# Kernel tuning notes

Hardware: AMD Instinct MI355X
Metric: run time of the kernel (lower is better)

Reference implementation:

```python
import jax, jax.numpy as jnp
import numpy as np

D_MODEL = 768
N_HEADS = 12
HEAD_DIM = D_MODEL // N_HEADS


def setup_inputs() -> dict:
    key = jax.random.key(0)
    ks = jax.random.split(key, 9)
    B, S = 2, 2048
    x = jax.random.normal(ks[0], (B, S, D_MODEL), dtype=jnp.float32)
    s = 1.0 / np.sqrt(D_MODEL)
    Wq = jax.random.normal(ks[1], (D_MODEL, D_MODEL), dtype=jnp.float32) * s
    bq = jax.random.normal(ks[2], (D_MODEL,), dtype=jnp.float32) * 0.01
    Wk = jax.random.normal(ks[3], (D_MODEL, D_MODEL), dtype=jnp.float32) * s
    bk = jax.random.normal(ks[4], (D_MODEL,), dtype=jnp.float32) * 0.01
    Wv = jax.random.normal(ks[5], (D_MODEL, D_MODEL), dtype=jnp.float32) * s
    bv = jax.random.normal(ks[6], (D_MODEL,), dtype=jnp.float32) * 0.01
    Wo = jax.random.normal(ks[7], (D_MODEL, D_MODEL), dtype=jnp.float32) * s
    bo = jax.random.normal(ks[8], (D_MODEL,), dtype=jnp.float32) * 0.01
    return {"x": x, "Wq": Wq, "bq": bq, "Wk": Wk, "bk": bk,
            "Wv": Wv, "bv": bv, "Wo": Wo, "bo": bo}


def reference(x, Wq, bq, Wk, bk, Wv, bv, Wo, bo):
    B, S, _ = x.shape
    H, Dh = N_HEADS, HEAD_DIM
    # Projections (torch Linear: x @ W.T + b; here W stored as [in, out])
    q = (x @ Wq + bq).reshape(B, S, H, Dh)
    k = (x @ Wk + bk).reshape(B, S, H, Dh)
    v = (x @ Wv + bv).reshape(B, S, H, Dh)
    scale = 1.0 / jnp.sqrt(jnp.float32(Dh))
    # NOTE: source applies no causal mask despite the class name.
    scores = jnp.einsum('bqhd,bkhd->bhqk', q, k) * scale
    attn = jax.nn.softmax(scores, axis=-1)
    out = jnp.einsum('bhqk,bkhd->bqhd', attn, v).reshape(B, S, H * Dh)
    return out @ Wo + bo
```

## Files before the change

kernel.cpp:

```cpp
#include <hip/hip_runtime.h>

typedef unsigned short u16;
typedef __fp16 halfx2 __attribute__((ext_vector_type(2)));
typedef __fp16 halfx8 __attribute__((ext_vector_type(8)));
typedef float floatx4 __attribute__((ext_vector_type(4)));
typedef unsigned short u16x4 __attribute__((ext_vector_type(4)));
typedef unsigned short u16x8 __attribute__((ext_vector_type(8)));

#define D_MODEL 768
#define NH 12
#define DH 64
#define SEQ 2048
#define BATCH 2
#define MTOK 4096
#define DQKV 2304

__device__ __forceinline__ u16 f2h(float f) {
    __fp16 h = (__fp16)f;
    return __builtin_bit_cast(u16, h);
}

__device__ __forceinline__ void gload_lds16(const void* g, void* l) {
    __builtin_amdgcn_global_load_lds(
        (const __attribute__((address_space(1))) void*)g,
        (__attribute__((address_space(3))) void*)l, 16, 0, 0);
}


__global__ __launch_bounds__(256) void wprep_kernel(const float* __restrict__ Wq, const float* __restrict__ Wk,
                                                    const float* __restrict__ Wv, const float* __restrict__ Wo,
                                                    const float* __restrict__ x,
                                                    u16* __restrict__ WqkvT, u16* __restrict__ WoT,
                                                    u16* __restrict__ xh) {
    __shared__ u16 t[64][72];
    int bid = blockIdx.x;
    int tid = threadIdx.x;
    if (bid >= 576) {
        int idx = (bid - 576) * 2048 + tid * 8;
        float4 v0 = *(const float4*)(x + idx);
        float4 v1 = *(const float4*)(x + idx + 4);
        union { u16x8 u; halfx2 h[4]; } pk;
        pk.h[0] = __builtin_amdgcn_cvt_pkrtz(v0.x, v0.y);
        pk.h[1] = __builtin_amdgcn_cvt_pkrtz(v0.z, v0.w);
        pk.h[2] = __builtin_amdgcn_cvt_pkrtz(v1.x, v1.y);
        pk.h[3] = __builtin_amdgcn_cvt_pkrtz(v1.z, v1.w);
        *(u16x8*)(xh + idx) = pk.u;
        return;
    }
    int z = bid / 144;
    int t2 = bid % 144;
    int k0 = (t2 / 12) * 64, n0 = (t2 % 12) * 64;
    const float* W = (z == 0) ? Wq : (z == 1) ? Wk : (z == 2) ? Wv : Wo;
    u16* dst = (z < 3) ? (WqkvT + (size_t)z * 768 * 768) : WoT;
#pragma unroll
    for (int p = 0; p < 16; ++p) {
        int idx = p * 256 + tid;
        int kr = idx >> 6, nc = idx & 63;
        t[kr][nc] = f2h(W[(size_t)(k0 + kr) * 768 + n0 + nc]);
    }
    __syncthreads();
#pragma unroll
    for (int p = 0; p < 16; ++p) {
        int idx = p * 256 + tid;
        int nr = idx >> 6, kc = idx & 63;
        dst[(size_t)(n0 + nr) * 768 + k0 + kc] = t[kc][nr];
    }
}


__global__ __launch_bounds__(256) void gemm_qkv(const u16* __restrict__ xh, const u16* __restrict__ Bt,
                                                const float* __restrict__ bq, const float* __restrict__ bk,
                                                const float* __restrict__ bv,
                                                u16* __restrict__ qP, u16* __restrict__ kP,
                                                u16* __restrict__ vTout) {
    const int tid = threadIdx.x;
    const int wid = tid >> 6;
    const int lane = tid & 63;
    const int qd = lane >> 4;
    const int l15 = lane & 15;

    const int tn = blockIdx.x * 128;
    const int tm = blockIdx.y * 64;
    const int wm = (wid >> 1) * 32;
    const int wn = (wid & 1) * 64;

    __shared__ alignas(16) u16 As[64 * 64];
    __shared__ alignas(16) u16 Bs[128 * 64];

    floatx4 acc[2][4];
#pragma unroll
    for (int i = 0; i < 2; ++i)
#pragma unroll
        for (int j = 0; j < 4; ++j) acc[i][j] = (floatx4)(0.0f);

    const u16* Ag[2];
#pragma unroll
    for (int rd = 0; rd < 2; ++rd) {
        int s = rd * 256 + tid;
        int r = s >> 3, bl = (s & 7) ^ (r & 7);
        Ag[rd] = xh + (size_t)(tm + r) * 768 + bl * 8;
    }
    const u16* Bg[4];
#pragma unroll
    for (int rd = 0; rd < 4; ++rd) {
        int s = rd * 256 + tid;
        int r = s >> 3, bl = (s & 7) ^ (r & 7);
        Bg[rd] = Bt + (size_t)(tn + r) * 768 + bl * 8;
    }

    for (int kb = 0; kb < 768; kb += 64) {
        __syncthreads();
#pragma unroll
        for (int rd = 0; rd < 2; ++rd)
            gload_lds16(Ag[rd] + kb, As + (size_t)(rd * 256 + tid) * 8);
#pragma unroll
        for (int rd = 0; rd < 4; ++rd)
            gload_lds16(Bg[rd] + kb, Bs + (size_t)(rd * 256 + tid) * 8);
        __syncthreads();

#pragma unroll
        for (int ks = 0; ks < 2; ++ks) {
            halfx8 af[2], bf[4];
#pragma unroll
            for (int i = 0; i < 2; ++i) {
                int r = wm + i * 16 + l15;
                af[i] = *(const halfx8*)(As + r * 64 + (((ks * 4 + qd) ^ (r & 7)) * 8));
            }
#pragma unroll
            for (int j = 0; j < 4; ++j) {
                int r2 = wn + j * 16 + l15;
                bf[j] = *(const halfx8*)(Bs + r2 * 64 + (((ks * 4 + qd) ^ (r2 & 7)) * 8));
            }
#pragma unroll
            for (int i = 0; i < 2; ++i)
#pragma unroll
                for (int j = 0; j < 4; ++j)
                    acc[i][j] = __builtin_amdgcn_mfma_f32_16x16x32_f16(af[i], bf[j], acc[i][j], 0, 0, 0);
        }
    }

    const float cscale = 0.125f * 1.44269504088896340736f;
    const int rgn = (tn < 768) ? 0 : (tn < 1536) ? 1 : 2;
    const float* bsrc = (rgn == 0) ? bq : (rgn == 1) ? bk : bv;
#pragma unroll
    for (int j = 0; j < 4; ++j) {
        int col = tn + wn + j * 16 + l15;
        int cl = col - rgn * 768;
        float bvv = bsrc[cl];
        int h = cl >> 6, d = cl & 63;
#pragma unroll
        for (int i = 0; i < 2; ++i) {
            int row0 = tm + wm + i * 16 + qd * 4;
            int b = row0 >> 11, s0 = row0 & 2047;
            u16x4 pk;
#pragma unroll
            for (int r = 0; r < 4; ++r) {
                float v = acc[i][j][r] + bvv;
                if (rgn == 0) v *= cscale;
                pk[r] = f2h(v);
            }
            if (rgn == 2) {
                *(u16x4*)(vTout + ((size_t)(b * NH + h) * 64 + d) * SEQ + s0) = pk;
            } else {
                u16* dst = (rgn == 0) ? qP : kP;
#pragma unroll
                for (int r = 0; r < 4; ++r)
                    dst[((size_t)(b * NH + h) * SEQ + s0 + r) * DH + d] = pk[r];
            }
        }
    }
}


__global__ __launch_bounds__(256, 3) void attn_kernel(const u16* __restrict__ qP, const u16* __restrict__ kP,
                                                      const u16* __restrict__ vT, u16* __restrict__ attn) {
    const int tid = threadIdx.x;
    const int wid = tid >> 6;
    const int lane = tid & 63;
    const int qd = lane >> 4;
    const int l15 = lane & 15;

    const int bh = blockIdx.x;
    const int b = bh / NH, h = bh % NH;
    const int q0 = blockIdx.y * 64;

    __shared__ alignas(16) u16 smem[13312];
    u16* qlds = smem;
    u16* ps = smem + 4096 + wid * 2304;

#pragma unroll
    for (int ks = 0; ks < 2; ++ks) {
        halfx8 qv = *(const halfx8*)(qP + (size_t)(bh * SEQ + q0 + wid * 16 + l15) * DH + ks * 32 + qd * 8);
        *(halfx8*)(qlds + (size_t)((ks * 4 + wid) * 64 + lane) * 8) = qv;
    }
    __syncthreads();

    auto AQ = [&](int jn, int ks) -> halfx8 {
        return *(const halfx8*)(qlds + (size_t)((ks * 4 + jn) * 64 + lane) * 8);
    };

    floatx4 o[4][4];
#pragma unroll
    for (int ip = 0; ip < 4; ++ip)
#pragma unroll
        for (int jn = 0; jn < 4; ++jn) o[ip][jn] = (floatx4)(0.0f);
    float lsum[4] = {0.0f, 0.0f, 0.0f, 0.0f};

    const u16* kbase = kP + (size_t)(bh * SEQ + wid * 32 + l15) * DH + qd * 8;
    const u16* vbase = vT + (size_t)(bh * 64 + l15) * SEQ + wid * 32 + qd * 8;

    floatx4 sc[2][4];
    {
        halfx8 ak0[2][2];
#pragma unroll
        for (int mi = 0; mi < 2; ++mi)
#pragma unroll
            for (int ks = 0; ks < 2; ++ks)
                ak0[mi][ks] = *(const halfx8*)(kbase + (size_t)(mi * 16) * DH + ks * 32);
#pragma unroll
        for (int jn = 0; jn < 4; ++jn) {
            halfx8 a0 = AQ(jn, 0), a1 = AQ(jn, 1);
#pragma unroll
            for (int mi = 0; mi < 2; ++mi) {
                floatx4 z = (floatx4)(0.0f);
                z = __builtin_amdgcn_mfma_f32_16x16x32_f16(ak0[mi][0], a0, z, 0, 0, 0);
                sc[mi][jn] = __builtin_amdgcn_mfma_f32_16x16x32_f16(ak0[mi][1], a1, z, 0, 0, 0);
            }
        }
    }

    for (int kt = 0; kt < 16; ++kt) {
        const int kt1 = (kt + 1) & 15;

        halfx8 akn[2][2];
#pragma unroll
        for (int mi = 0; mi < 2; ++mi)
#pragma unroll
            for (int ks = 0; ks < 2; ++ks)
                akn[mi][ks] = *(const halfx8*)(kbase + (size_t)(kt1 * 128 + mi * 16) * DH + ks * 32);
        halfx8 avc[4];
#pragma unroll
        for (int ip = 0; ip < 4; ++ip)
            avc[ip] = *(const halfx8*)(vbase + (size_t)(ip * 16) * SEQ + kt * 128);

#pragma unroll
        for (int mi = 0; mi < 2; ++mi)
#pragma unroll
            for (int jn = 0; jn < 4; ++jn) {
                float p0 = __builtin_amdgcn_exp2f(sc[mi][jn][0]);
                float p1 = __builtin_amdgcn_exp2f(sc[mi][jn][1]);
                float p2 = __builtin_amdgcn_exp2f(sc[mi][jn][2]);
                float p3 = __builtin_amdgcn_exp2f(sc[mi][jn][3]);
                lsum[jn] += (p0 + p1) + (p2 + p3);
                union { u16x4 u; halfx2 h[2]; } pk;
                pk.h[0] = __builtin_amdgcn_cvt_pkrtz(p0, p1);
                pk.h[1] = __builtin_amdgcn_cvt_pkrtz(p2, p3);
                *(u16x4*)(ps + (jn * 16 + l15) * 36 + mi * 16 + qd * 4) = pk.u;
            }

        __builtin_amdgcn_s_setprio(1);
#pragma unroll
        for (int jn = 0; jn < 4; ++jn) {
            halfx8 a0 = AQ(jn, 0), a1 = AQ(jn, 1);
#pragma unroll
            for (int mi = 0; mi < 2; ++mi) {
                floatx4 z = (floatx4)(0.0f);
                z = __builtin_amdgcn_mfma_f32_16x16x32_f16(akn[mi][0], a0, z, 0, 0, 0);
                sc[mi][jn] = __builtin_amdgcn_mfma_f32_16x16x32_f16(akn[mi][1], a1, z, 0, 0, 0);
            }
        }
        __builtin_amdgcn_s_setprio(0);

#pragma unroll
        for (int jn = 0; jn < 4; ++jn) {
            union { halfx8 h8; u16x4 u4[2]; } bpu;
            bpu.u4[0] = *(const u16x4*)(ps + (jn * 16 + l15) * 36 + qd * 8);
            bpu.u4[1] = *(const u16x4*)(ps + (jn * 16 + l15) * 36 + qd * 8 + 4);
            __builtin_amdgcn_s_setprio(1);
#pragma unroll
            for (int ip = 0; ip < 4; ++ip)
                o[ip][jn] = __builtin_amdgcn_mfma_f32_16x16x32_f16(avc[ip], bpu.h8, o[ip][jn], 0, 0, 0);
            __builtin_amdgcn_s_setprio(0);
        }
    }

#pragma unroll
    for (int jn = 0; jn < 4; ++jn) {
        float v = lsum[jn];
        v += __shfl_xor(v, 16, 64);
        v += __shfl_xor(v, 32, 64);
        lsum[jn] = v;
    }

    float* Oacc = (float*)smem;
    float* la = (float*)smem + 4352;

    __syncthreads();
    if (wid == 0) {
#pragma unroll
        for (int jn = 0; jn < 4; ++jn) {
            int q = jn * 16 + l15;
#pragma unroll
            for (int ip = 0; ip < 4; ++ip)
                *(floatx4*)(Oacc + q * 68 + ip * 16 + qd * 4) = o[ip][jn];
            if (qd == 0) la[q] = lsum[jn];
        }
    }
    for (int w = 1; w < 4; ++w) {
        __syncthreads();
        if (wid == w) {
#pragma unroll
            for (int jn = 0; jn < 4; ++jn) {
                int q = jn * 16 + l15;
#pragma unroll
                for (int ip = 0; ip < 4; ++ip) {
                    float* p = Oacc + q * 68 + ip * 16 + qd * 4;
                    *(floatx4*)p = *(floatx4*)p + o[ip][jn];
                }
                if (qd == 0) la[q] += lsum[jn];
            }
        }
    }
    __syncthreads();

    {
        int q = tid >> 2, d0 = (tid & 3) * 16;
        float inv = __builtin_amdgcn_rcpf(la[q]);
        const float* op = Oacc + q * 68 + d0;
        u16x8 pk0, pk1;
#pragma unroll
        for (int r = 0; r < 8; ++r) pk0[r] = f2h(op[r] * inv);
#pragma unroll
        for (int r = 0; r < 8; ++r) pk1[r] = f2h(op[8 + r] * inv);
        u16* dst = attn + (size_t)(b * SEQ + q0 + q) * D_MODEL + h * DH + d0;
        *(u16x8*)dst = pk0;
        *(u16x8*)(dst + 8) = pk1;
    }
}


__global__ __launch_bounds__(256) void gemm_out(const u16* __restrict__ A, const u16* __restrict__ Bt,
                                                const float* __restrict__ bias, float* __restrict__ Cout) {
    const int tid = threadIdx.x;
    const int wid = tid >> 6;
    const int lane = tid & 63;
    const int qd = lane >> 4;
    const int l15 = lane & 15;

    const int tn = blockIdx.x * 64;
    const int tm = blockIdx.y * 64;
    const int wm = (wid >> 1) * 32;
    const int wn = (wid & 1) * 32;

    __shared__ alignas(16) u16 As[64 * 64];
    __shared__ alignas(16) u16 Bs[64 * 64];

    floatx4 acc[2][2];
#pragma unroll
    for (int i = 0; i < 2; ++i)
#pragma unroll
        for (int j = 0; j < 2; ++j) acc[i][j] = (floatx4)(0.0f);

    const u16* Ag[2];
    const u16* Bg[2];
#pragma unroll
    for (int rd = 0; rd < 2; ++rd) {
        int s = rd * 256 + tid;
        int r = s >> 3, bl = (s & 7) ^ (r & 7);
        Ag[rd] = A + (size_t)(tm + r) * 768 + bl * 8;
        Bg[rd] = Bt + (size_t)(tn + r) * 768 + bl * 8;
    }

    for (int kb = 0; kb < 768; kb += 64) {
        __syncthreads();
#pragma unroll
        for (int rd = 0; rd < 2; ++rd) {
            gload_lds16(Ag[rd] + kb, As + (size_t)(rd * 256 + tid) * 8);
            gload_lds16(Bg[rd] + kb, Bs + (size_t)(rd * 256 + tid) * 8);
        }
        __syncthreads();

#pragma unroll
        for (int ks = 0; ks < 2; ++ks) {
            halfx8 af[2], bf[2];
#pragma unroll
            for (int i = 0; i < 2; ++i) {
                int r = wm + i * 16 + l15;
                af[i] = *(const halfx8*)(As + r * 64 + (((ks * 4 + qd) ^ (r & 7)) * 8));
                int r2 = wn + i * 16 + l15;
                bf[i] = *(const halfx8*)(Bs + r2 * 64 + (((ks * 4 + qd) ^ (r2 & 7)) * 8));
            }
#pragma unroll
            for (int i = 0; i < 2; ++i)
#pragma unroll
                for (int j = 0; j < 2; ++j)
                    acc[i][j] = __builtin_amdgcn_mfma_f32_16x16x32_f16(af[i], bf[j], acc[i][j], 0, 0, 0);
        }
    }

#pragma unroll
    for (int j = 0; j < 2; ++j) {
        int col = tn + wn + j * 16 + l15;
        float bv = bias[col];
#pragma unroll
        for (int i = 0; i < 2; ++i) {
            int row0 = tm + wm + i * 16 + qd * 4;
#pragma unroll
            for (int r = 0; r < 4; ++r)
                Cout[(size_t)(row0 + r) * 768 + col] = acc[i][j][r] + bv;
        }
    }
}


extern "C" void kernel_launch(void* const* d_in, const int* in_sizes, int n_in,
                              void* d_out, int out_size, void* d_ws, size_t ws_size,
                              hipStream_t stream) {
    const float* x  = (const float*)d_in[0];
    const float* Wq = (const float*)d_in[1];
    const float* bq = (const float*)d_in[2];
    const float* Wk = (const float*)d_in[3];
    const float* bk = (const float*)d_in[4];
    const float* Wv = (const float*)d_in[5];
    const float* bv = (const float*)d_in[6];
    const float* Wo = (const float*)d_in[7];
    const float* bo = (const float*)d_in[8];

    char* ws = (char*)d_ws;
    size_t off = 0;
    auto take = [&](size_t bytes) -> char* {
        char* p = ws + off;
        off += (bytes + 255) & ~(size_t)255;
        return p;
    };
    u16* WqkvT = (u16*)take((size_t)DQKV * D_MODEL * 2);
    u16* WoT   = (u16*)take((size_t)D_MODEL * D_MODEL * 2);
    u16* qP    = (u16*)take((size_t)MTOK * D_MODEL * 2);
    u16* kP    = (u16*)take((size_t)MTOK * D_MODEL * 2);
    u16* vTb   = (u16*)take((size_t)BATCH * NH * DH * SEQ * 2);
    u16* attn  = (u16*)take((size_t)MTOK * D_MODEL * 2);
    u16* xh = attn;

    wprep_kernel<<<576 + (MTOK * D_MODEL / 2048), 256, 0, stream>>>(Wq, Wk, Wv, Wo, x, WqkvT, WoT, xh);
    gemm_qkv<<<dim3(DQKV / 128, MTOK / 64), 256, 0, stream>>>(xh, WqkvT, bq, bk, bv, qP, kP, vTb);
    attn_kernel<<<dim3(BATCH * NH, SEQ / 64), 256, 0, stream>>>(qP, kP, vTb, attn);
    gemm_out<<<dim3(D_MODEL / 64, MTOK / 64), 256, 0, stream>>>(attn, WoT, bo, (float*)d_out);
}
```

Measured before the change: 197.5 us.

## Stage GEMM epilogues through LDS, swizzle block order, vectorize weight transpose

Both GEMM epilogues now write results into shared memory and then issue coalesced vector stores (16-byte rows for q/k, 4-wide for vT, float4 for output) instead of scattered 2-byte or 4-byte stores. The launch grids become 1D with an XCD-aware block swizzle (bid&7 strides), meant to improve L2 locality across the MI355X chiplets. The weight-prep kernel reads float4 and writes u16x2 with a narrower padded tile. The attention loop is marked unroll 1 to cut code size and register pressure. The cost is extra LDS traffic, more syncs, and possible bank conflicts in the new LDS access patterns.

```diff
diff --git a/kernel.cpp b/kernel.cpp
--- a/kernel.cpp
+++ b/kernel.cpp
@@ -4,6 +4,7 @@
 typedef __fp16 halfx2 __attribute__((ext_vector_type(2)));
 typedef __fp16 halfx8 __attribute__((ext_vector_type(8)));
 typedef float floatx4 __attribute__((ext_vector_type(4)));
+typedef unsigned short u16x2 __attribute__((ext_vector_type(2)));
 typedef unsigned short u16x4 __attribute__((ext_vector_type(4)));
 typedef unsigned short u16x8 __attribute__((ext_vector_type(8)));
 
@@ -32,7 +33,7 @@
                                                     const float* __restrict__ x,
                                                     u16* __restrict__ WqkvT, u16* __restrict__ WoT,
                                                     u16* __restrict__ xh) {
-    __shared__ u16 t[64][72];
+    __shared__ u16 t[64][66];
     int bid = blockIdx.x;
     int tid = threadIdx.x;
     if (bid >= 576) {
@@ -52,18 +53,24 @@
     int k0 = (t2 / 12) * 64, n0 = (t2 % 12) * 64;
     const float* W = (z == 0) ? Wq : (z == 1) ? Wk : (z == 2) ? Wv : Wo;
     u16* dst = (z < 3) ? (WqkvT + (size_t)z * 768 * 768) : WoT;
-#pragma unroll
-    for (int p = 0; p < 16; ++p) {
+
+#pragma unroll
+    for (int p = 0; p < 4; ++p) {
         int idx = p * 256 + tid;
-        int kr = idx >> 6, nc = idx & 63;
-        t[kr][nc] = f2h(W[(size_t)(k0 + kr) * 768 + n0 + nc]);
-    }
-    __syncthreads();
-#pragma unroll
-    for (int p = 0; p < 16; ++p) {
+        int kr = idx >> 4, nq = (idx & 15) * 4;
+        float4 v = *(const float4*)(W + (size_t)(k0 + kr) * 768 + n0 + nq);
+        t[nq + 0][kr] = f2h(v.x);
+        t[nq + 1][kr] = f2h(v.y);
+        t[nq + 2][kr] = f2h(v.z);
+        t[nq + 3][kr] = f2h(v.w);
+    }
+    __syncthreads();
+#pragma unroll
+    for (int p = 0; p < 8; ++p) {
         int idx = p * 256 + tid;
-        int nr = idx >> 6, kc = idx & 63;
-        dst[(size_t)(n0 + nr) * 768 + k0 + kc] = t[kc][nr];
+        int nr = idx >> 5, c2 = (idx & 31) * 2;
+        u16x2 v = *(const u16x2*)(&t[nr][c2]);
+        *(u16x2*)(dst + (size_t)(n0 + nr) * 768 + k0 + c2) = v;
     }
 }
 
@@ -79,13 +86,16 @@
     const int qd = lane >> 4;
     const int l15 = lane & 15;
 
-    const int tn = blockIdx.x * 128;
-    const int tm = blockIdx.y * 64;
+    const int bid = blockIdx.x;
+    const int swz = (bid & 7) * 144 + (bid >> 3);
+    const int tn = (swz % 18) * 128;
+    const int tm = (swz / 18) * 64;
     const int wm = (wid >> 1) * 32;
     const int wn = (wid & 1) * 64;
 
-    __shared__ alignas(16) u16 As[64 * 64];
-    __shared__ alignas(16) u16 Bs[128 * 64];
+    __shared__ alignas(16) u16 sm[12288];
+    u16* As = sm;
+    u16* Bs = sm + 4096;
 
     floatx4 acc[2][4];
 #pragma unroll
@@ -142,31 +152,51 @@
     const float cscale = 0.125f * 1.44269504088896340736f;
     const int rgn = (tn < 768) ? 0 : (tn < 1536) ? 1 : 2;
     const float* bsrc = (rgn == 0) ? bq : (rgn == 1) ? bk : bv;
+
+    __syncthreads();
+    u16* T = sm;
+
 #pragma unroll
     for (int j = 0; j < 4; ++j) {
-        int col = tn + wn + j * 16 + l15;
-        int cl = col - rgn * 768;
+        int col = wn + j * 16 + l15;
+        int cl = tn + col - rgn * 768;
         float bvv = bsrc[cl];
-        int h = cl >> 6, d = cl & 63;
 #pragma unroll
         for (int i = 0; i < 2; ++i) {
-            int row0 = tm + wm + i * 16 + qd * 4;
-            int b = row0 >> 11, s0 = row0 & 2047;
-            u16x4 pk;
+            int row0 = wm + i * 16 + qd * 4;
 #pragma unroll
             for (int r = 0; r < 4; ++r) {
                 float v = acc[i][j][r] + bvv;
                 if (rgn == 0) v *= cscale;
-                pk[r] = f2h(v);
-            }
-            if (rgn == 2) {
-                *(u16x4*)(vTout + ((size_t)(b * NH + h) * 64 + d) * SEQ + s0) = pk;
-            } else {
-                u16* dst = (rgn == 0) ? qP : kP;
-#pragma unroll
-                for (int r = 0; r < 4; ++r)
-                    dst[((size_t)(b * NH + h) * SEQ + s0 + r) * DH + d] = pk[r];
-            }
+                T[(size_t)(row0 + r) * 132 + col] = f2h(v);
+            }
+        }
+    }
+    __syncthreads();
+
+    const int hbase = (tn - rgn * 768) >> 6;
+    const int b = tm >> 11, s0 = tm & 2047;
+
+    if (rgn < 2) {
+        u16* dst = (rgn == 0) ? qP : kP;
+#pragma unroll
+        for (int it = 0; it < 4; ++it) {
+            int idx = it * 256 + tid;
+            int token = idx >> 4, rem = idx & 15;
+            int hh = rem >> 3, sub = rem & 7;
+            u16x8 v = *(const u16x8*)(T + (size_t)token * 132 + hh * 64 + sub * 8);
+            *(u16x8*)(dst + ((size_t)(b * NH + hbase + hh) * SEQ + s0 + token) * DH + sub * 8) = v;
+        }
+    } else {
+#pragma unroll
+        for (int it = 0; it < 8; ++it) {
+            int idx = it * 256 + tid;
+            int c = idx >> 4, tq = (idx & 15) * 4;
+            u16x4 v;
+#pragma unroll
+            for (int k = 0; k < 4; ++k) v[k] = T[(size_t)(tq + k) * 132 + c];
+            int h = hbase + (c >> 6), d = c & 63;
+            *(u16x4*)(vTout + ((size_t)(b * NH + h) * 64 + d) * SEQ + s0 + tq) = v;
         }
     }
 }
@@ -229,6 +259,7 @@
         }
     }
 
+#pragma unroll 1
     for (int kt = 0; kt < 16; ++kt) {
         const int kt1 = (kt + 1) & 15;
 
@@ -347,13 +378,16 @@
     const int qd = lane >> 4;
     const int l15 = lane & 15;
 
-    const int tn = blockIdx.x * 64;
-    const int tm = blockIdx.y * 64;
+    const int bid = blockIdx.x;
+    const int swz = (bid & 7) * 96 + (bid >> 3);
+    const int tn = (swz % 12) * 64;
+    const int tm = (swz / 12) * 64;
     const int wm = (wid >> 1) * 32;
     const int wn = (wid & 1) * 32;
 
-    __shared__ alignas(16) u16 As[64 * 64];
-    __shared__ alignas(16) u16 Bs[64 * 64];
+    __shared__ alignas(16) u16 sm[8704];
+    u16* As = sm;
+    u16* Bs = sm + 4096;
 
     floatx4 acc[2][2];
 #pragma unroll
@@ -398,17 +432,29 @@
         }
     }
 
+    __syncthreads();
+    float* T = (float*)sm;
+
 #pragma unroll
     for (int j = 0; j < 2; ++j) {
-        int col = tn + wn + j * 16 + l15;
-        float bv = bias[col];
+        int col = wn + j * 16 + l15;
+        float bv = bias[tn + col];
 #pragma unroll
         for (int i = 0; i < 2; ++i) {
-            int row0 = tm + wm + i * 16 + qd * 4;
+            int row0 = wm + i * 16 + qd * 4;
 #pragma unroll
             for (int r = 0; r < 4; ++r)
-                Cout[(size_t)(row0 + r) * 768 + col] = acc[i][j][r] + bv;
-        }
+                T[(size_t)(row0 + r) * 66 + col] = acc[i][j][r] + bv;
+        }
+    }
+    __syncthreads();
+
+#pragma unroll
+    for (int it = 0; it < 4; ++it) {
+        int idx = it * 256 + tid;
+        int row = idx >> 4, c4 = (idx & 15) * 4;
+        floatx4 v = *(const floatx4*)(T + (size_t)row * 66 + c4);
+        *(floatx4*)(Cout + (size_t)(tm + row) * 768 + tn + c4) = v;
     }
 }
 
@@ -442,7 +488,7 @@
     u16* xh = attn;
 
     wprep_kernel<<<576 + (MTOK * D_MODEL / 2048), 256, 0, stream>>>(Wq, Wk, Wv, Wo, x, WqkvT, WoT, xh);
-    gemm_qkv<<<dim3(DQKV / 128, MTOK / 64), 256, 0, stream>>>(xh, WqkvT, bq, bk, bv, qP, kP, vTb);
+    gemm_qkv<<<1152, 256, 0, stream>>>(xh, WqkvT, bq, bk, bv, qP, kP, vTb);
     attn_kernel<<<dim3(BATCH * NH, SEQ / 64), 256, 0, stream>>>(qP, kP, vTb, attn);
-    gemm_out<<<dim3(D_MODEL / 64, MTOK / 64), 256, 0, stream>>>(attn, WoT, bo, (float*)d_out);
-}
+    gemm_out<<<768, 256, 0, stream>>>(attn, WoT, bo, (float*)d_out);
+}
```

Result: no change. 195.6 us (-0.9%).
